# Performance work log

Hardware: AMD Instinct MI355X
Metric: run time of the kernel (lower is better)

Reference implementation:

```python
import jax, jax.numpy as jnp
import numpy as np

N_EMBED = 1024
HEAD_SIZE = 64
BLOCK_SIZE = 2048


def setup_inputs() -> dict:
    key = jax.random.key(0)
    kx, kk, kv = jax.random.split(key, 3)
    x = jax.random.normal(kx, (8, 2048, N_EMBED), dtype=jnp.float32)
    # nn.Linear(n_embed, head_size, bias=False): weight [head_size, n_embed]
    scale = 1.0 / np.sqrt(N_EMBED)
    W_k = jax.random.uniform(kk, (HEAD_SIZE, N_EMBED), dtype=jnp.float32, minval=-scale, maxval=scale)
    W_v = jax.random.uniform(kv, (HEAD_SIZE, N_EMBED), dtype=jnp.float32, minval=-scale, maxval=scale)
    return {"x": x, "W_k": W_k, "W_v": W_v}


def reference(x, W_k, W_v):
    # Faithful to source: q = self.key(x) (query projection is unused in the original forward)
    T = x.shape[1]
    k = jnp.einsum('btc,hc->bth', x, W_k)   # [B,T,H]
    q = k                                    # source bug: q uses key projection
    wei = jnp.einsum('bth,bsh->bts', q, k) * (HEAD_SIZE ** -0.5)  # [B,T,T]
    causal = jnp.tril(jnp.ones((T, T), dtype=bool))
    wei = jnp.where(causal, wei, -jnp.inf)
    wei = jax.nn.softmax(wei, axis=-1)
    v = jnp.einsum('btc,hc->bth', x, W_v)
    out = jnp.einsum('bts,bsh->bth', wei, v)
    return out
```

## Files before the change

kernel.cpp:

```cpp
#include <hip/hip_runtime.h>


typedef __bf16 bf16;
typedef __bf16 bf16x4 __attribute__((ext_vector_type(4)));
typedef __bf16 bf16x8 __attribute__((ext_vector_type(8)));
typedef float  floatx4 __attribute__((ext_vector_type(4)));

#define T_LEN 2048
#define HEAD  64
#define CEMB  1024

static __device__ __forceinline__ void async16(const void* g, void* l) {
    __builtin_amdgcn_global_load_lds(
        (const __attribute__((address_space(1))) void*)g,
        (__attribute__((address_space(3))) void*)l, 16, 0, 0);
}

static __device__ __forceinline__ bf16x8 cvt2(float4 a, float4 b) {
    bf16x8 r;
    r[0] = (bf16)a.x; r[1] = (bf16)a.y; r[2] = (bf16)a.z; r[3] = (bf16)a.w;
    r[4] = (bf16)b.x; r[5] = (bf16)b.y; r[6] = (bf16)b.z; r[7] = (bf16)b.w;
    return r;
}
static __device__ __forceinline__ bf16x4 cvt1(float4 a) {
    bf16x4 r;
    r[0] = (bf16)a.x; r[1] = (bf16)a.y; r[2] = (bf16)a.z; r[3] = (bf16)a.w;
    return r;
}

__global__ __launch_bounds__(256) void wconv_kernel(const float* __restrict__ Wk,
                                                    const float* __restrict__ Wv,
                                                    bf16* __restrict__ Wb) {
    int i = (blockIdx.x * 256 + threadIdx.x) * 4;
    const float* src = (i < 64 * 1024) ? (Wk + i) : (Wv + (i - 64 * 1024));
    *(bf16x4*)&Wb[i] = cvt1(*(const float4*)src);
}

__global__ __launch_bounds__(256) void proj_kernel(const float* __restrict__ x,
                                                   const bf16* __restrict__ Wb,
                                                   bf16* __restrict__ Kbuf,
                                                   bf16* __restrict__ Vt) {
    __shared__ __align__(16) float As[2][32 * 64];
    __shared__ __align__(16) bf16  Bs[2][128 * 64];

    const int tid  = threadIdx.x;
    const int wave = tid >> 6;
    const int lane = tid & 63;
    const int quad = lane >> 4;
    const int low  = lane & 15;

    const long row0 = (long)blockIdx.x * 32;

    const int ar_ = lane >> 4;
    const int ac_ = (lane & 15) ^ (wave * 4 + ar_);
    const int br_ = lane >> 3;
    const int bc_ = (lane & 7) ^ br_;

    const int strip = wave & 1;
    const int nq    = (wave >> 1) * 4;

    floatx4 acc[4];
#pragma unroll
    for (int i = 0; i < 4; ++i) acc[i] = (floatx4){0.f, 0.f, 0.f, 0.f};

    auto stage = [&](int s, int sb) {
        const int k0 = s * 64;
#pragma unroll
        for (int m = 0; m < 2; ++m) {
            const int r = (m * 4 + wave) * 4 + ar_;
            async16(x + (row0 + r) * CEMB + k0 + ac_ * 4, &As[sb][(m * 4 + wave) * 256]);
        }
#pragma unroll
        for (int m = 0; m < 4; ++m) {
            const int r = (m * 4 + wave) * 8 + br_;
            async16(Wb + r * CEMB + k0 + bc_ * 8, &Bs[sb][(m * 4 + wave) * 512]);
        }
    };

    stage(0, 0);
    stage(1, 1);
    __syncthreads();

    int buf = 0;
    for (int s = 0; s < 16; ++s) {
#pragma unroll
        for (int ks = 0; ks < 2; ++ks) {
            const int rr = strip * 16 + low;
            const int c0 = ks * 8 + quad * 2;
            float4 a0 = *(const float4*)&As[buf][rr * 64 + ((c0 ^ low) * 4)];
            float4 a1 = *(const float4*)&As[buf][rr * 64 + (((c0 + 1) ^ low) * 4)];
            bf16x8 afrag = cvt2(a0, a1);
            const int cq = ks * 4 + quad;
#pragma unroll
            for (int i = 0; i < 4; ++i) {
                const int r2 = (nq + i) * 16 + low;
                bf16x8 bfrag = *(const bf16x8*)&Bs[buf][r2 * 64 + ((cq ^ (low & 7)) * 8)];
                acc[i] = __builtin_amdgcn_mfma_f32_16x16x32_bf16(afrag, bfrag, acc[i], 0, 0, 0);
            }
        }
        if (s < 15) {
            __syncthreads();
            if (s < 14) stage(s + 2, buf);
            buf ^= 1;
        }
    }

    __syncthreads();
    bf16* Ek = (bf16*)&Bs[0][0];
    bf16* Ev = (bf16*)&Bs[1][0];
    if (wave < 2) {
#pragma unroll
        for (int i = 0; i < 4; ++i)
#pragma unroll
            for (int r = 0; r < 4; ++r)
                Ek[(strip * 16 + quad * 4 + r) * 72 + i * 16 + low] = (bf16)acc[i][r];
    } else {
#pragma unroll
        for (int i = 0; i < 4; ++i)
#pragma unroll
            for (int r = 0; r < 4; ++r)
                Ev[(i * 16 + low) * 36 + strip * 16 + quad * 4 + r] = (bf16)acc[i][r];
    }
    __syncthreads();

    const long bidx  = row0 >> 11;
    const int  tloc0 = (int)(row0 & 2047);
    {
        const int t  = tid >> 3;
        const int h0 = (tid & 7) * 8;
        *(bf16x8*)&Kbuf[(bidx * T_LEN + tloc0 + t) * HEAD + h0] = *(const bf16x8*)&Ek[t * 72 + h0];
    }
    {
        const int h  = tid >> 2;
        const int t0 = (tid & 3) * 8;
        *(bf16x8*)&Vt[(bidx * HEAD + h) * T_LEN + tloc0 + t0] = *(const bf16x8*)&Ev[h * 36 + t0];
    }
}

__global__ __launch_bounds__(256) void attn_kernel(const bf16* __restrict__ Kbuf,
                                                   const bf16* __restrict__ Vt,
                                                   bf16* __restrict__ Opart,
                                                   float* __restrict__ lpart) {
    __shared__ __align__(16) bf16 Ks[2][64 * 64];
    __shared__ __align__(16) bf16 Vs[2][64 * 64];
    __shared__ __align__(16) bf16 Ps[4][16][72];

    const int tid  = threadIdx.x;
    const int wave = tid >> 6;
    const int lane = tid & 63;
    const int quad = lane >> 4;
    const int low  = lane & 15;

    const int c  = blockIdx.x & 3;
    const int qb = (blockIdx.x >> 2) & 31;
    const int b  = blockIdx.x >> 7;

    const bf16* kbase = Kbuf + (long)b * T_LEN * HEAD;
    const bf16* vbase = Vt + (long)b * HEAD * T_LEN;

    const bf16* qrow = kbase + (qb * 64 + wave * 16 + low) * HEAD + quad * 8;
    const bf16x8 qf0 = *(const bf16x8*)(qrow);
    const bf16x8 qf1 = *(const bf16x8*)(qrow + 32);

    bf16x8 ones;
#pragma unroll
    for (int i = 0; i < 8; ++i) ones[i] = (bf16)1.0f;

    floatx4 o[4], ol;
#pragma unroll
    for (int nt = 0; nt < 4; ++nt) o[nt] = (floatx4){0.f, 0.f, 0.f, 0.f};
    ol = (floatx4){0.f, 0.f, 0.f, 0.f};

    const int br_ = lane >> 3;
    const int bc_ = (lane & 7) ^ br_;

    auto stage = [&](int j, int sb) {
#pragma unroll
        for (int m = 0; m < 2; ++m) {
            const int r = (m * 4 + wave) * 8 + br_;
            async16(kbase + (j * 64 + r) * HEAD + bc_ * 8, &Ks[sb][(m * 4 + wave) * 512]);
            async16(vbase + (long)r * T_LEN + j * 64 + bc_ * 8, &Vs[sb][(m * 4 + wave) * 512]);
        }
    };

    if (c <= qb) {
        stage(c, 0);
        if (c + 4 <= qb) stage(c + 4, 1);
        __syncthreads();

        int buf = 0;
        for (int j = c; j <= qb; j += 4) {
            floatx4 s_[4];
#pragma unroll
            for (int nt = 0; nt < 4; ++nt) {
                const int r2 = nt * 16 + low;
                bf16x8 kf0 = *(const bf16x8*)&Ks[buf][r2 * 64 + ((quad ^ (low & 7)) * 8)];
                bf16x8 kf1 = *(const bf16x8*)&Ks[buf][r2 * 64 + (((4 + quad) ^ (low & 7)) * 8)];
                floatx4 z = (floatx4){0.f, 0.f, 0.f, 0.f};
                z = __builtin_amdgcn_mfma_f32_16x16x32_bf16(qf0, kf0, z, 0, 0, 0);
                z = __builtin_amdgcn_mfma_f32_16x16x32_bf16(qf1, kf1, z, 0, 0, 0);
                s_[nt] = z;
            }

            const bool diag = (j == qb);
#pragma unroll
            for (int nt = 0; nt < 4; ++nt) {
#pragma unroll
                for (int r = 0; r < 4; ++r) {
                    float p = __builtin_amdgcn_exp2f(s_[nt][r] * 0.180336880f);
                    if (diag && (nt * 16 + low) > (wave * 16 + quad * 4 + r)) p = 0.f;
                    Ps[wave][quad * 4 + r][nt * 16 + low] = (bf16)p;
                }
            }

            bf16x8 pf0 = *(const bf16x8*)&Ps[wave][low][quad * 8];
            bf16x8 pf1 = *(const bf16x8*)&Ps[wave][low][32 + quad * 8];
#pragma unroll
            for (int nt = 0; nt < 4; ++nt) {
                const int r2 = nt * 16 + low;
                bf16x8 vf0 = *(const bf16x8*)&Vs[buf][r2 * 64 + ((quad ^ (low & 7)) * 8)];
                bf16x8 vf1 = *(const bf16x8*)&Vs[buf][r2 * 64 + (((4 + quad) ^ (low & 7)) * 8)];
                o[nt] = __builtin_amdgcn_mfma_f32_16x16x32_bf16(pf0, vf0, o[nt], 0, 0, 0);
                o[nt] = __builtin_amdgcn_mfma_f32_16x16x32_bf16(pf1, vf1, o[nt], 0, 0, 0);
            }
            ol = __builtin_amdgcn_mfma_f32_16x16x32_bf16(pf0, ones, ol, 0, 0, 0);
            ol = __builtin_amdgcn_mfma_f32_16x16x32_bf16(pf1, ones, ol, 0, 0, 0);

            if (j + 4 <= qb) {
                __syncthreads();
                if (j + 8 <= qb) stage(j + 8, buf);
                buf ^= 1;
            }
        }
    }

    __syncthreads();
    bf16* Eo = (bf16*)&Ks[0][0];
#pragma unroll
    for (int nt = 0; nt < 4; ++nt)
#pragma unroll
        for (int r = 0; r < 4; ++r)
            Eo[(wave * 16 + quad * 4 + r) * 72 + nt * 16 + low] = (bf16)o[nt][r];
    __syncthreads();
    {
        const int row  = tid >> 2;
        const int col0 = (tid & 3) * 16;
        bf16* ob = Opart + (long)blockIdx.x * 4096 + row * 64 + col0;
        *(bf16x8*)(ob)     = *(const bf16x8*)&Eo[row * 72 + col0];
        *(bf16x8*)(ob + 8) = *(const bf16x8*)&Eo[row * 72 + col0 + 8];
    }
    if (low == 0) {
#pragma unroll
        for (int r = 0; r < 4; ++r)
            lpart[(long)blockIdx.x * 64 + wave * 16 + quad * 4 + r] = ol[r];
    }
}

__global__ __launch_bounds__(256) void attn_combine(const bf16* __restrict__ Opart,
                                                    const float* __restrict__ lpart,
                                                    float* __restrict__ out) {
    const int tile = blockIdx.x;
    const int tid  = threadIdx.x;
    const int row  = tid >> 2;
    const int col0 = (tid & 3) * 16;

    const bf16*  ob = Opart + (long)tile * 4 * 4096 + row * 64 + col0;
    const float* lb = lpart + (long)tile * 4 * 64 + row;

    float l = lb[0] + lb[64] + lb[128] + lb[192];
    float rl = 1.0f / l;

    float s[16];
#pragma unroll
    for (int i = 0; i < 16; ++i) s[i] = 0.f;
#pragma unroll
    for (int ch = 0; ch < 4; ++ch) {
        bf16x8 u0 = *(const bf16x8*)(ob + ch * 4096);
        bf16x8 u1 = *(const bf16x8*)(ob + ch * 4096 + 8);
#pragma unroll
        for (int i = 0; i < 8; ++i) { s[i] += (float)u0[i]; s[8 + i] += (float)u1[i]; }
    }
    float4* op = (float4*)(out + (long)tile * 4096 + row * 64 + col0);
#pragma unroll
    for (int v = 0; v < 4; ++v) {
        float4 w;
        w.x = s[v * 4 + 0] * rl; w.y = s[v * 4 + 1] * rl;
        w.z = s[v * 4 + 2] * rl; w.w = s[v * 4 + 3] * rl;
        op[v] = w;
    }
}

extern "C" void kernel_launch(void* const* d_in, const int* in_sizes, int n_in,
                              void* d_out, int out_size, void* d_ws, size_t ws_size,
                              hipStream_t stream) {
    const float* x  = (const float*)d_in[0];
    const float* Wk = (const float*)d_in[1];
    const float* Wv = (const float*)d_in[2];
    float* out = (float*)d_out;

    char* ws = (char*)d_ws;
    bf16*  Wb    = (bf16*)ws;
    bf16*  Kbuf  = (bf16*)(ws + (1 << 20));
    bf16*  Vt    = (bf16*)(ws + (3 << 20));
    bf16*  Opart = (bf16*)(ws + (5 << 20));
    float* lpart = (float*)(ws + (13 << 20));

    wconv_kernel<<<128, 256, 0, stream>>>(Wk, Wv, Wb);
    proj_kernel<<<512, 256, 0, stream>>>(x, Wb, Kbuf, Vt);
    attn_kernel<<<1024, 256, 0, stream>>>(Kbuf, Vt, Opart, lpart);
    attn_combine<<<256, 256, 0, stream>>>(Opart, lpart, out);
}
```

Measured before the change: 131.3 us.

## Split causal attention into balanced 128x128 query/key tile-pair blocks

Work is redistributed so each block handles a pair of 64-row query tiles against a pair of 64-row key tiles, enumerating only the lower-triangular (J,P) pairs, 136 per batch. This replaces the earlier 4-way strided key split, where the block count and the work per block were uneven. Each block stages its K/V tiles once and reuses them for two query tiles. The cost is up to 16 partial outputs per query tile, which means more Opart/lpart traffic and a longer combine loop, plus a larger workspace.

```diff
diff --git a/kernel.cpp b/kernel.cpp
--- a/kernel.cpp
+++ b/kernel.cpp
@@ -151,54 +151,64 @@
     const int quad = lane >> 4;
     const int low  = lane & 15;
 
-    const int c  = blockIdx.x & 3;
-    const int qb = (blockIdx.x >> 2) & 31;
-    const int b  = blockIdx.x >> 7;
+    int t = blockIdx.x % 136;
+    const int b = blockIdx.x / 136;
+    int J = 0;
+    while (t >= 16 - J) { t -= 16 - J; ++J; }
+    const int P = J + t;
 
     const bf16* kbase = Kbuf + (long)b * T_LEN * HEAD;
     const bf16* vbase = Vt + (long)b * HEAD * T_LEN;
 
-    const bf16* qrow = kbase + (qb * 64 + wave * 16 + low) * HEAD + quad * 8;
-    const bf16x8 qf0 = *(const bf16x8*)(qrow);
-    const bf16x8 qf1 = *(const bf16x8*)(qrow + 32);
-
-    bf16x8 ones;
-#pragma unroll
-    for (int i = 0; i < 8; ++i) ones[i] = (bf16)1.0f;
-
-    floatx4 o[4], ol;
-#pragma unroll
-    for (int nt = 0; nt < 4; ++nt) o[nt] = (floatx4){0.f, 0.f, 0.f, 0.f};
-    ol = (floatx4){0.f, 0.f, 0.f, 0.f};
+    bf16x8 qf[2][2];
+#pragma unroll
+    for (int tq = 0; tq < 2; ++tq) {
+        const bf16* qrow = kbase + ((2 * P + tq) * 64 + wave * 16 + low) * HEAD + quad * 8;
+        qf[tq][0] = *(const bf16x8*)(qrow);
+        qf[tq][1] = *(const bf16x8*)(qrow + 32);
+    }
 
     const int br_ = lane >> 3;
     const int bc_ = (lane & 7) ^ br_;
-
-    auto stage = [&](int j, int sb) {
+#pragma unroll
+    for (int jj = 0; jj < 2; ++jj) {
+        const int j = 2 * J + jj;
 #pragma unroll
         for (int m = 0; m < 2; ++m) {
             const int r = (m * 4 + wave) * 8 + br_;
-            async16(kbase + (j * 64 + r) * HEAD + bc_ * 8, &Ks[sb][(m * 4 + wave) * 512]);
-            async16(vbase + (long)r * T_LEN + j * 64 + bc_ * 8, &Vs[sb][(m * 4 + wave) * 512]);
-        }
-    };
-
-    if (c <= qb) {
-        stage(c, 0);
-        if (c + 4 <= qb) stage(c + 4, 1);
-        __syncthreads();
-
-        int buf = 0;
-        for (int j = c; j <= qb; j += 4) {
+            async16(kbase + (j * 64 + r) * HEAD + bc_ * 8, &Ks[jj][(m * 4 + wave) * 512]);
+            async16(vbase + (long)r * T_LEN + j * 64 + bc_ * 8, &Vs[jj][(m * 4 + wave) * 512]);
+        }
+    }
+    __syncthreads();
+
+    bf16x8 ones;
+#pragma unroll
+    for (int i = 0; i < 8; ++i) ones[i] = (bf16)1.0f;
+
+#pragma unroll
+    for (int tq = 0; tq < 2; ++tq) {
+        const int qb = 2 * P + tq;
+
+        floatx4 o[4], ol;
+#pragma unroll
+        for (int nt = 0; nt < 4; ++nt) o[nt] = (floatx4){0.f, 0.f, 0.f, 0.f};
+        ol = (floatx4){0.f, 0.f, 0.f, 0.f};
+
+#pragma unroll
+        for (int jj = 0; jj < 2; ++jj) {
+            const int j = 2 * J + jj;
+            if (j > qb) continue;
+
             floatx4 s_[4];
 #pragma unroll
             for (int nt = 0; nt < 4; ++nt) {
                 const int r2 = nt * 16 + low;
-                bf16x8 kf0 = *(const bf16x8*)&Ks[buf][r2 * 64 + ((quad ^ (low & 7)) * 8)];
-                bf16x8 kf1 = *(const bf16x8*)&Ks[buf][r2 * 64 + (((4 + quad) ^ (low & 7)) * 8)];
+                bf16x8 kf0 = *(const bf16x8*)&Ks[jj][r2 * 64 + ((quad ^ (low & 7)) * 8)];
+                bf16x8 kf1 = *(const bf16x8*)&Ks[jj][r2 * 64 + (((4 + quad) ^ (low & 7)) * 8)];
                 floatx4 z = (floatx4){0.f, 0.f, 0.f, 0.f};
-                z = __builtin_amdgcn_mfma_f32_16x16x32_bf16(qf0, kf0, z, 0, 0, 0);
-                z = __builtin_amdgcn_mfma_f32_16x16x32_bf16(qf1, kf1, z, 0, 0, 0);
+                z = __builtin_amdgcn_mfma_f32_16x16x32_bf16(qf[tq][0], kf0, z, 0, 0, 0);
+                z = __builtin_amdgcn_mfma_f32_16x16x32_bf16(qf[tq][1], kf1, z, 0, 0, 0);
                 s_[nt] = z;
             }
 
@@ -218,41 +228,35 @@
 #pragma unroll
             for (int nt = 0; nt < 4; ++nt) {
                 const int r2 = nt * 16 + low;
-                bf16x8 vf0 = *(const bf16x8*)&Vs[buf][r2 * 64 + ((quad ^ (low & 7)) * 8)];
-                bf16x8 vf1 = *(const bf16x8*)&Vs[buf][r2 * 64 + (((4 + quad) ^ (low & 7)) * 8)];
+                bf16x8 vf0 = *(const bf16x8*)&Vs[jj][r2 * 64 + ((quad ^ (low & 7)) * 8)];
+                bf16x8 vf1 = *(const bf16x8*)&Vs[jj][r2 * 64 + (((4 + quad) ^ (low & 7)) * 8)];
                 o[nt] = __builtin_amdgcn_mfma_f32_16x16x32_bf16(pf0, vf0, o[nt], 0, 0, 0);
                 o[nt] = __builtin_amdgcn_mfma_f32_16x16x32_bf16(pf1, vf1, o[nt], 0, 0, 0);
             }
             ol = __builtin_amdgcn_mfma_f32_16x16x32_bf16(pf0, ones, ol, 0, 0, 0);
             ol = __builtin_amdgcn_mfma_f32_16x16x32_bf16(pf1, ones, ol, 0, 0, 0);
-
-            if (j + 4 <= qb) {
-                __syncthreads();
-                if (j + 8 <= qb) stage(j + 8, buf);
-                buf ^= 1;
-            }
-        }
-    }
-
-    __syncthreads();
-    bf16* Eo = (bf16*)&Ks[0][0];
-#pragma unroll
-    for (int nt = 0; nt < 4; ++nt)
-#pragma unroll
-        for (int r = 0; r < 4; ++r)
-            Eo[(wave * 16 + quad * 4 + r) * 72 + nt * 16 + low] = (bf16)o[nt][r];
-    __syncthreads();
-    {
-        const int row  = tid >> 2;
-        const int col0 = (tid & 3) * 16;
-        bf16* ob = Opart + (long)blockIdx.x * 4096 + row * 64 + col0;
-        *(bf16x8*)(ob)     = *(const bf16x8*)&Eo[row * 72 + col0];
-        *(bf16x8*)(ob + 8) = *(const bf16x8*)&Eo[row * 72 + col0 + 8];
-    }
-    if (low == 0) {
-#pragma unroll
-        for (int r = 0; r < 4; ++r)
-            lpart[(long)blockIdx.x * 64 + wave * 16 + quad * 4 + r] = ol[r];
+        }
+
+        bf16* Eo = (bf16*)&Ps[wave][0][0];
+#pragma unroll
+        for (int nt = 0; nt < 4; ++nt)
+#pragma unroll
+            for (int r = 0; r < 4; ++r)
+                Eo[(quad * 4 + r) * 72 + nt * 16 + low] = (bf16)o[nt][r];
+
+        const long pidx = ((long)(b * 32 + qb) * 16 + J);
+        {
+            const int rr   = lane >> 2;
+            const int col0 = (lane & 3) * 16;
+            bf16* ob = Opart + pidx * 4096 + (wave * 16 + rr) * 64 + col0;
+            *(bf16x8*)(ob)     = *(const bf16x8*)&Eo[rr * 72 + col0];
+            *(bf16x8*)(ob + 8) = *(const bf16x8*)&Eo[rr * 72 + col0 + 8];
+        }
+        if (low == 0) {
+#pragma unroll
+            for (int r = 0; r < 4; ++r)
+                lpart[pidx * 64 + wave * 16 + quad * 4 + r] = ol[r];
+        }
     }
 }
 
@@ -260,23 +264,23 @@
                                                     const float* __restrict__ lpart,
                                                     float* __restrict__ out) {
     const int tile = blockIdx.x;
+    const int qb   = tile & 31;
+    const int nJ   = (qb >> 1) + 1;
     const int tid  = threadIdx.x;
     const int row  = tid >> 2;
     const int col0 = (tid & 3) * 16;
 
-    const bf16*  ob = Opart + (long)tile * 4 * 4096 + row * 64 + col0;
-    const float* lb = lpart + (long)tile * 4 * 64 + row;
-
-    float l = lb[0] + lb[64] + lb[128] + lb[192];
+    float l = 0.f;
+    for (int ch = 0; ch < nJ; ++ch) l += lpart[((long)tile * 16 + ch) * 64 + row];
     float rl = 1.0f / l;
 
     float s[16];
 #pragma unroll
     for (int i = 0; i < 16; ++i) s[i] = 0.f;
-#pragma unroll
-    for (int ch = 0; ch < 4; ++ch) {
-        bf16x8 u0 = *(const bf16x8*)(ob + ch * 4096);
-        bf16x8 u1 = *(const bf16x8*)(ob + ch * 4096 + 8);
+    for (int ch = 0; ch < nJ; ++ch) {
+        const bf16* ob = Opart + ((long)tile * 16 + ch) * 4096 + row * 64 + col0;
+        bf16x8 u0 = *(const bf16x8*)(ob);
+        bf16x8 u1 = *(const bf16x8*)(ob + 8);
 #pragma unroll
         for (int i = 0; i < 8; ++i) { s[i] += (float)u0[i]; s[8 + i] += (float)u1[i]; }
     }
@@ -303,10 +307,10 @@
     bf16*  Kbuf  = (bf16*)(ws + (1 << 20));
     bf16*  Vt    = (bf16*)(ws + (3 << 20));
     bf16*  Opart = (bf16*)(ws + (5 << 20));
-    float* lpart = (float*)(ws + (13 << 20));
+    float* lpart = (float*)(ws + (40 << 20));
 
     wconv_kernel<<<128, 256, 0, stream>>>(Wk, Wv, Wb);
     proj_kernel<<<512, 256, 0, stream>>>(x, Wb, Kbuf, Vt);
-    attn_kernel<<<1024, 256, 0, stream>>>(Kbuf, Vt, Opart, lpart);
+    attn_kernel<<<8 * 136, 256, 0, stream>>>(Kbuf, Vt, Opart, lpart);
     attn_combine<<<256, 256, 0, stream>>>(Opart, lpart, out);
 }
```

After: 134.6 us. 2.5% more time.
